# Kernel optimization log

Measured on AMD Instinct MI355X. Metric: run time of the kernel, lower is better.

The kernel has to match this reference:

```python
import jax, jax.numpy as jnp
import numpy as np
from math import sqrt

B, T, C = 4, 2048, 2048
H = 16
D = C // H  # head_dim = 128


def setup_inputs() -> dict:
    key = jax.random.key(0)
    ks = jax.random.split(key, 7)
    s = 1.0 / sqrt(C)
    return {
        "querys": jax.random.normal(ks[0], (B, T, C), dtype=jnp.float32),
        "keys": jax.random.normal(ks[1], (B, T, C), dtype=jnp.float32),
        "values": jax.random.normal(ks[2], (B, T, C), dtype=jnp.float32),
        "Wq": jax.random.normal(ks[3], (C, C), dtype=jnp.float32) * s,
        "bq": jnp.zeros((C,), dtype=jnp.float32),
        "Wk": jax.random.normal(ks[4], (C, C), dtype=jnp.float32) * s,
        "bk": jnp.zeros((C,), dtype=jnp.float32),
        "Wv": jax.random.normal(ks[5], (C, C), dtype=jnp.float32) * s,
        "bv": jnp.zeros((C,), dtype=jnp.float32),
        "Wo": jax.random.normal(ks[6], (C, C), dtype=jnp.float32) * s,
        "bo": jnp.zeros((C,), dtype=jnp.float32),
        "is_causal": 1,
    }


def reference(querys, keys, values, Wq, bq, Wk, bk, Wv, bv, Wo, bo, is_causal):
    # Linear projections: x @ W^T + b (torch nn.Linear convention), here W stored as [C_in, C_out]
    q = (querys @ Wq + bq).reshape(B, T, H, D)
    k = (keys @ Wk + bk).reshape(B, T, H, D)
    v = (values @ Wv + bv).reshape(B, T, H, D)
    # scores: [B, H, T, T]
    scores = jnp.einsum("bqhd,bkhd->bhqk", q, k) / sqrt(D)
    if is_causal:
        mask = jnp.tril(jnp.ones((T, T), dtype=bool))  # allowed positions
        scores = jnp.where(mask, scores, -jnp.inf)
    weights = jax.nn.softmax(scores, axis=-1)
    attn = jnp.einsum("bhqk,bkhd->bqhd", weights, v).reshape(B, T, C)
    return attn @ Wo + bo
```

## Files before the change

kernel.cpp:

```cpp
#include <hip/hip_runtime.h>
#include <hip/hip_bf16.h>
#include <stdint.h>

#define BB 4
#define TT 2048
#define CC 2048
#define HH 16
#define DD 128
#define MM (BB*TT)

typedef __attribute__((ext_vector_type(8))) short bh8;
typedef __attribute__((ext_vector_type(4))) float fx4;

__device__ inline ushort f2bf(float x) {
    union { float f; uint32_t u; } c; c.f = x;
    uint32_t lsb = (c.u >> 16) & 1u;
    return (ushort)((c.u + 0x7fffu + lsb) >> 16);
}

__device__ inline void async16(const void* g, void* l) {
    __builtin_amdgcn_global_load_lds(
        (const __attribute__((address_space(1))) uint32_t*)g,
        (__attribute__((address_space(3))) uint32_t*)l, 16, 0, 0);
}

__global__ __launch_bounds__(256) void convert3_k(
    const float* __restrict__ i0, const float* __restrict__ i1,
    const float* __restrict__ i2,
    ushort* __restrict__ o0, ushort* __restrict__ o1, ushort* __restrict__ o2,
    int n)
{
    const float* in; ushort* out;
    switch (blockIdx.y) {
        case 0:  in = i0; out = o0; break;
        case 1:  in = i1; out = o1; break;
        default: in = i2; out = o2; break;
    }
    int i = (int)(blockIdx.x * 256 + threadIdx.x) * 4;
    if (i + 3 < n) {
        float4 v = *(const float4*)&in[i];
        ushort4 o;
        o.x = f2bf(v.x); o.y = f2bf(v.y); o.z = f2bf(v.z); o.w = f2bf(v.w);
        *(ushort4*)&out[i] = o;
    }
}

__global__ __launch_bounds__(256) void transpose4_w_k(
    const float* __restrict__ w0, const float* __restrict__ w1,
    const float* __restrict__ w2, const float* __restrict__ w3,
    ushort* __restrict__ t0, ushort* __restrict__ t1,
    ushort* __restrict__ t2, ushort* __restrict__ t3)
{
    const float* W; ushort* Wt;
    switch (blockIdx.z) {
        case 0:  W = w0; Wt = t0; break;
        case 1:  W = w1; Wt = t1; break;
        case 2:  W = w2; Wt = t2; break;
        default: W = w3; Wt = t3; break;
    }
    __shared__ __align__(16) ushort tile[32][33];
    const int n0 = blockIdx.x * 32, k0 = blockIdx.y * 32;
    const int tx = threadIdx.x, ty = threadIdx.y;
#pragma unroll
    for (int r = 0; r < 32; r += 8)
        tile[ty + r][tx] = f2bf(W[(size_t)(k0 + ty + r) * CC + n0 + tx]);
    __syncthreads();
    const int tid = ty * 32 + tx;
    const int p = tid & 15;
    const int row = tid >> 4;
#pragma unroll
    for (int rr = 0; rr < 2; ++rr) {
        const int n_row = row + rr * 16;
        ushort2 w2;
        w2.x = tile[2 * p][n_row];
        w2.y = tile[2 * p + 1][n_row];
        *(ushort2*)&Wt[(size_t)(n0 + n_row) * CC + k0 + 2 * p] = w2;
    }
}

__global__ __launch_bounds__(256) void transpose_v_k(
    const ushort* __restrict__ V, ushort* __restrict__ Vt)
{
    __shared__ __align__(16) ushort tile[32][33];
    const int bh = blockIdx.z;
    const int b = bh >> 4, h = bh & 15;
    const int t0 = blockIdx.y * 32, d0 = blockIdx.x * 32;
    const int tx = threadIdx.x, ty = threadIdx.y;
    const ushort* Vp = V + (size_t)b * TT * CC + h * DD;
#pragma unroll
    for (int r = 0; r < 32; r += 8)
        tile[ty + r][tx] = Vp[(size_t)(t0 + ty + r) * CC + d0 + tx];
    __syncthreads();
    ushort* Vtp = Vt + (size_t)bh * DD * TT;
    const int tt = t0 + tx;
    const int p64 = (tt & ~63) | (((tt & 15) << 2) | ((tt >> 4) & 3));
#pragma unroll
    for (int r = 0; r < 32; r += 8)
        Vtp[(size_t)(d0 + ty + r) * TT + p64] = tile[tx][ty + r];
}

template<int OUTF>
__global__ __launch_bounds__(512, 2) void gemm_bf16_k(
    const ushort* __restrict__ A, const ushort* __restrict__ Bt,
    const float* __restrict__ bias, void* __restrict__ Cv, float osc)
{
    __shared__ __align__(16) char Gsm[2][65536];

    const int tid = (int)threadIdx.x;
    const int lane = tid & 63, wave = tid >> 6;
    const int fr = lane & 15, fg = lane >> 4;
    const int wm = wave >> 2, wn = wave & 3;

    const int n_tile = (int)blockIdx.x & 7;
    const int m_tile = (int)blockIdx.x >> 3;
    const int m0 = m_tile * 256, n0 = n_tile * 256;

    const ushort* Ag = A  + (size_t)m0 * CC;
    const ushort* Bg = Bt + (size_t)n0 * CC;
    const int nt = CC / 64;

    auto STAGE_G = [&](int t, int g) {
        if (t >= nt) return;
        const int khalf = g >> 1, isB = g & 1;
        char* base = Gsm[t & 1] + isB * 32768 + khalf * 16384;
        const ushort* src = isB ? Bg : Ag;
        const int kbase = t * 64 + khalf * 32;
#pragma unroll
        for (int l = 0; l < 2; ++l) {
            const int u = l * 512 + tid;
            const int j = u >> 3, s = u & 7;
            const int ek = s ^ (j & 7);
            const int e = (ek >> 2) & 1, ks = ek & 3;
            async16(src + (size_t)(2 * j + e) * CC + kbase + ks * 8,
                    base + u * 16);
        }
    };

    const int slot = ((((fr & 1) << 2) | fg) ^ ((fr >> 1) & 7));
    const int offA = (wm * 64 + (fr >> 1)) * 128 + slot * 16;
    const int offB = 32768 + (wn * 32 + (fr >> 1)) * 128 + slot * 16;

    fx4 acc[8][4];
#pragma unroll
    for (int i = 0; i < 8; ++i)
#pragma unroll
        for (int j = 0; j < 4; ++j)
            acc[i][j] = (fx4){0.f, 0.f, 0.f, 0.f};

#pragma unroll
    for (int g = 0; g < 4; ++g) STAGE_G(0, g);

#pragma unroll 1
    for (int t = 0; t < nt; ++t) {
        const char* kb = Gsm[t & 1];
#pragma unroll
        for (int kk = 0; kk < 2; ++kk) {
            if (t == nt - 1 && kk == 1) {
                asm volatile("s_waitcnt vmcnt(0)" ::: "memory");
            } else {
                asm volatile("s_waitcnt vmcnt(4)" ::: "memory");
            }
            __builtin_amdgcn_sched_barrier(0);
            __builtin_amdgcn_s_barrier();
            __builtin_amdgcn_sched_barrier(0);

            const char* ka = kb + kk * 16384;
            const char* kbB = kb + kk * 16384;
            bh8 afr[4], bfr[4];

#pragma unroll
            for (int nf = 0; nf < 4; ++nf)
                bfr[nf] = *(const bh8*)(kbB + offB + nf * 1024);
#pragma unroll
            for (int i = 0; i < 4; ++i)
                afr[i] = *(const bh8*)(ka + offA + i * 1024);
            STAGE_G(t + 1, kk * 2);

            __builtin_amdgcn_sched_barrier(0);
            __builtin_amdgcn_s_barrier();
            __builtin_amdgcn_sched_barrier(0);

            __builtin_amdgcn_s_setprio(1);
#pragma unroll
            for (int i = 0; i < 4; ++i)
#pragma unroll
                for (int nf = 0; nf < 4; ++nf)
                    acc[i][nf] = __builtin_amdgcn_mfma_f32_16x16x32_bf16(
                        afr[i], bfr[nf], acc[i][nf], 0, 0, 0);
            __builtin_amdgcn_s_setprio(0);

#pragma unroll
            for (int i = 0; i < 4; ++i)
                afr[i] = *(const bh8*)(ka + offA + (4 + i) * 1024);
            STAGE_G(t + 1, kk * 2 + 1);

            __builtin_amdgcn_sched_barrier(0);
            __builtin_amdgcn_s_barrier();
            __builtin_amdgcn_sched_barrier(0);

            __builtin_amdgcn_s_setprio(1);
#pragma unroll
            for (int i = 0; i < 4; ++i)
#pragma unroll
                for (int nf = 0; nf < 4; ++nf)
                    acc[4 + i][nf] = __builtin_amdgcn_mfma_f32_16x16x32_bf16(
                        afr[i], bfr[nf], acc[4 + i][nf], 0, 0, 0);
            __builtin_amdgcn_s_setprio(0);
        }
    }

#pragma unroll
    for (int nf = 0; nf < 4; ++nf) {
        const int col = n0 + wn * 64 + nf * 16 + fr;
        const float bv = bias[col];
#pragma unroll
        for (int mf = 0; mf < 8; ++mf) {
            const int row = m0 + wm * 128 + mf * 16 + fg * 4;
#pragma unroll
            for (int r = 0; r < 4; ++r) {
                float v = (acc[mf][nf][r] + bv) * osc;
                if (OUTF)
                    ((float*)Cv)[(size_t)(row + r) * CC + col] = v;
                else
                    ((ushort*)Cv)[(size_t)(row + r) * CC + col] = f2bf(v);
            }
        }
    }
}

__global__ __launch_bounds__(512, 4) void flash_attn_k(
    const ushort* __restrict__ Qm, const ushort* __restrict__ Km,
    const ushort* __restrict__ Vt, ushort* __restrict__ Om,
    const int* __restrict__ causal_p)
{
    __shared__ __align__(16) char Ksm[2][16384];
    __shared__ __align__(16) char Vsm[2][16384];
    __shared__ __align__(16) char Psm[8][2048];

    const int tid = (int)threadIdx.x;
    const int lane = tid & 63, wave = tid >> 6;
    const int fr = lane & 15, fg = lane >> 4;
    const int causal = causal_p[0];

    const int d_raw = (int)blockIdx.x + 8 * ((int)blockIdx.y + 16 * (int)blockIdx.z);
    const int xcd = d_raw & 7, jj = d_raw >> 3;
    const int head_lin = xcd * 8 + (jj & 7);
    const int pi = jj >> 3;
    const int h = head_lin & 15, b = head_lin >> 4;

    const ushort* Qp = Qm + (size_t)b * TT * CC + h * DD;
    const ushort* Kp = Km + (size_t)b * TT * CC + h * DD;
    const ushort* Vp = Vt + (size_t)(b * HH + h) * DD * TT;
    ushort* Op = Om + (size_t)b * TT * CC + h * DD;
    char* pl = Psm[wave];

    auto STAGE = [&](int ti, int buf) {
        const int kv0 = ti * 64;
        {
            const int r0 = tid >> 4, s0 = tid & 15;
            async16(Kp + (size_t)(kv0 + r0) * CC + (s0 ^ (r0 & 15)) * 8,
                    Ksm[buf] + tid * 16);
            async16(Kp + (size_t)(kv0 + 32 + r0) * CC + (s0 ^ (r0 & 15)) * 8,
                    Ksm[buf] + 8192 + tid * 16);
        }
        {
            const int d0 = tid >> 3, s0 = tid & 7;
            async16(Vp + (size_t)d0 * TT + kv0 + (s0 ^ (d0 & 7)) * 8,
                    Vsm[buf] + tid * 16);
            async16(Vp + (size_t)(64 + d0) * TT + kv0 + (s0 ^ (d0 & 7)) * 8,
                    Vsm[buf] + 8192 + tid * 16);
        }
    };

#pragma unroll 1
    for (int pp = 0; pp < 2; ++pp) {
        const int tile = pp ? (15 - pi) : pi;
        const int q0 = tile * 128;
        const int qbase = q0 + wave * 16;

        bh8 qf[4];
#pragma unroll
        for (int s = 0; s < 4; ++s)
            qf[s] = *(const bh8*)&Qp[(size_t)(qbase + fr) * CC + s * 32 + fg * 8];

        fx4 o[8];
#pragma unroll
        for (int jn = 0; jn < 8; ++jn) o[jn] = (fx4){0.f, 0.f, 0.f, 0.f};
        float l_r[4] = {0.f, 0.f, 0.f, 0.f};

        const int nfull  = causal ? (q0 >> 6) : (TT / 64);
        const int ntiles = causal ? (nfull + 2) : (TT / 64);

        STAGE(0, 0);
#pragma unroll 1
        for (int t = 0; t < ntiles; ++t) {
            const bool last = (t == ntiles - 1);
            if (!last) STAGE(t + 1, (t + 1) & 1);
            if (!last) { asm volatile("s_waitcnt vmcnt(4)" ::: "memory"); }
            else       { asm volatile("s_waitcnt vmcnt(0)" ::: "memory"); }
            __builtin_amdgcn_sched_barrier(0);
            __builtin_amdgcn_s_barrier();
            __builtin_amdgcn_sched_barrier(0);

            const int kv0 = t * 64;
            const char* kb = Ksm[t & 1];
            const char* vb = Vsm[t & 1];
            const bool domask = causal && (t >= nfull);
            const bool active = !domask || (kv0 <= qbase + 15);

            if (active) {
                fx4 s4[4];
#pragma unroll
                for (int j = 0; j < 4; ++j) s4[j] = (fx4){0.f, 0.f, 0.f, 0.f};
#pragma unroll
                for (int st = 0; st < 4; ++st) {
                    bh8 kf[4];
#pragma unroll
                    for (int j = 0; j < 4; ++j)
                        kf[j] = *(const bh8*)(kb + (j * 16 + fr) * 256 +
                                              ((st * 64 + fg * 16) ^ (fr << 4)));
#pragma unroll
                    for (int j = 0; j < 4; ++j)
                        s4[j] = __builtin_amdgcn_mfma_f32_16x16x32_bf16(
                            qf[st], kf[j], s4[j], 0, 0, 0);
                }

#pragma unroll
                for (int r = 0; r < 4; ++r) {
                    const int row = fg * 4 + r;
                    const int q_idx = qbase + row;
                    float pv[4];
#pragma unroll
                    for (int j = 0; j < 4; ++j) {
                        float v = s4[j][r];
                        if (domask && (kv0 + j * 16 + fr > q_idx)) v = -1e30f;
                        pv[j] = exp2f(v);
                        l_r[r] += pv[j];
                    }
                    uint w0, w1;
                    asm("v_cvt_pk_bf16_f32 %0, %1, %2"
                        : "=v"(w0) : "v"(pv[0]), "v"(pv[1]));
                    asm("v_cvt_pk_bf16_f32 %0, %1, %2"
                        : "=v"(w1) : "v"(pv[2]), "v"(pv[3]));
                    uint2 w2; w2.x = w0; w2.y = w1;
                    *(uint2*)(pl + row * 128 + ((fr * 8) ^ ((row & 7) << 4))) = w2;
                }

#pragma unroll
                for (int g = 0; g < 2; ++g) {
                    bh8 pf = *(const bh8*)(pl + fr * 128 +
                                           ((g * 64 + fg * 16) ^ ((fr & 7) << 4)));
#pragma unroll
                    for (int jn = 0; jn < 8; ++jn) {
                        bh8 vf = *(const bh8*)(vb + (jn * 16 + fr) * 128 +
                                               ((g * 64 + fg * 16) ^ ((fr & 7) << 4)));
                        o[jn] = __builtin_amdgcn_mfma_f32_16x16x32_bf16(
                            pf, vf, o[jn], 0, 0, 0);
                    }
                }
            }

            __builtin_amdgcn_sched_barrier(0);
            __builtin_amdgcn_s_barrier();
            __builtin_amdgcn_sched_barrier(0);
        }

#pragma unroll
        for (int r = 0; r < 4; ++r) {
            float l = l_r[r];
            l += __shfl_xor(l, 1, 16);
            l += __shfl_xor(l, 2, 16);
            l += __shfl_xor(l, 4, 16);
            l += __shfl_xor(l, 8, 16);
            l_r[r] = l;
        }

#pragma unroll
        for (int r = 0; r < 4; ++r) {
            const float inv = 1.0f / l_r[r];
            const size_t rowoff = (size_t)(qbase + fg * 4 + r) * CC;
#pragma unroll
            for (int jn = 0; jn < 8; ++jn)
                Op[rowoff + jn * 16 + fr] = f2bf(o[jn][r] * inv);
        }
    }
}

extern "C" void kernel_launch(void* const* d_in, const int* in_sizes, int n_in,
                              void* d_out, int out_size, void* d_ws, size_t ws_size,
                              hipStream_t stream)
{
    (void)in_sizes; (void)n_in; (void)out_size;
    const float* querys = (const float*)d_in[0];
    const float* keys   = (const float*)d_in[1];
    const float* values = (const float*)d_in[2];
    const float* Wq = (const float*)d_in[3];
    const float* bq = (const float*)d_in[4];
    const float* Wk = (const float*)d_in[5];
    const float* bk = (const float*)d_in[6];
    const float* Wv = (const float*)d_in[7];
    const float* bv = (const float*)d_in[8];
    const float* Wo = (const float*)d_in[9];
    const float* bo = (const float*)d_in[10];
    const int* is_causal = (const int*)d_in[11];

    const size_t WBYTES = (size_t)CC * CC * 2;
    const size_t XBYTES = (size_t)MM * CC * 2;
    if (ws_size < 4 * WBYTES + 4 * XBYTES) return;

    uint8_t* ws = (uint8_t*)d_ws;
    ushort* WqT = (ushort*)(ws);
    ushort* WkT = (ushort*)(ws + WBYTES);
    ushort* WvT = (ushort*)(ws + 2 * WBYTES);
    ushort* WoT = (ushort*)(ws + 3 * WBYTES);
    uint8_t* act = ws + 4 * WBYTES;
    ushort* Xq = (ushort*)(act);
    ushort* Xk = (ushort*)(act + XBYTES);
    ushort* Xv = (ushort*)(act + 2 * XBYTES);
    ushort* Qb = (ushort*)(act + 3 * XBYTES);
    ushort* Kb = Xq;
    ushort* Vb = Xk;
    ushort* Vt = Xv;
    ushort* Ob = Xk;

    dim3 tb(32, 8);
    transpose4_w_k<<<dim3(CC / 32, CC / 32, 4), tb, 0, stream>>>(
        Wq, Wk, Wv, Wo, WqT, WkT, WvT, WoT);

    const int nX = MM * CC;
    convert3_k<<<dim3(nX / 4 / 256, 3), 256, 0, stream>>>(
        querys, keys, values, Xq, Xk, Xv, nX);

    dim3 gg((MM / 256) * (CC / 256));

    const float QSC = 0.12751789836306614f;

    gemm_bf16_k<0><<<gg, 512, 0, stream>>>(Xq, WqT, bq, Qb, QSC);
    gemm_bf16_k<0><<<gg, 512, 0, stream>>>(Xk, WkT, bk, Kb, 1.0f);
    gemm_bf16_k<0><<<gg, 512, 0, stream>>>(Xv, WvT, bv, Vb, 1.0f);

    dim3 gvt(DD / 32, TT / 32, BB * HH);
    transpose_v_k<<<gvt, tb, 0, stream>>>(Vb, Vt);

    dim3 ga(8, HH, BB);
    flash_attn_k<<<ga, 512, 0, stream>>>(Qb, Kb, Vt, Ob, is_causal);

    gemm_bf16_k<1><<<gg, 512, 0, stream>>>(Ob, WoT, bo, d_out, 1.0f);
}
```

Baseline: 528.7 us.

## Compute transposed S so P stays in registers, dropping LDS round-trip

```diff
diff --git a/kernel.cpp b/kernel.cpp
--- a/kernel.cpp
+++ b/kernel.cpp
@@ -93,10 +93,10 @@
     __syncthreads();
     ushort* Vtp = Vt + (size_t)bh * DD * TT;
     const int tt = t0 + tx;
-    const int p64 = (tt & ~63) | (((tt & 15) << 2) | ((tt >> 4) & 3));
+    const int pnew = (tt & ~31) | (((tt >> 2) & 3) << 3) | (((tt >> 4) & 1) << 2) | (tt & 3);
 #pragma unroll
     for (int r = 0; r < 32; r += 8)
-        Vtp[(size_t)(d0 + ty + r) * TT + p64] = tile[tx][ty + r];
+        Vtp[(size_t)(d0 + ty + r) * TT + pnew] = tile[tx][ty + r];
 }
 
 template<int OUTF>
@@ -235,7 +235,6 @@
 {
     __shared__ __align__(16) char Ksm[2][16384];
     __shared__ __align__(16) char Vsm[2][16384];
-    __shared__ __align__(16) char Psm[8][2048];
 
     const int tid = (int)threadIdx.x;
     const int lane = tid & 63, wave = tid >> 6;
@@ -252,7 +251,6 @@
     const ushort* Kp = Km + (size_t)b * TT * CC + h * DD;
     const ushort* Vp = Vt + (size_t)(b * HH + h) * DD * TT;
     ushort* Op = Om + (size_t)b * TT * CC + h * DD;
-    char* pl = Psm[wave];
 
     auto STAGE = [&](int ti, int buf) {
         const int kv0 = ti * 64;
@@ -277,6 +275,7 @@
         const int tile = pp ? (15 - pi) : pi;
         const int q0 = tile * 128;
         const int qbase = q0 + wave * 16;
+        const int q_idx = qbase + fr;
 
         bh8 qf[4];
 #pragma unroll
@@ -286,7 +285,7 @@
         fx4 o[8];
 #pragma unroll
         for (int jn = 0; jn < 8; ++jn) o[jn] = (fx4){0.f, 0.f, 0.f, 0.f};
-        float l_r[4] = {0.f, 0.f, 0.f, 0.f};
+        float l_acc = 0.f;
 
         const int nfull  = causal ? (q0 >> 6) : (TT / 64);
         const int ntiles = causal ? (nfull + 2) : (TT / 64);
@@ -312,6 +311,7 @@
                 fx4 s4[4];
 #pragma unroll
                 for (int j = 0; j < 4; ++j) s4[j] = (fx4){0.f, 0.f, 0.f, 0.f};
+                __builtin_amdgcn_s_setprio(1);
 #pragma unroll
                 for (int st = 0; st < 4; ++st) {
                     bh8 kf[4];
@@ -322,34 +322,37 @@
 #pragma unroll
                     for (int j = 0; j < 4; ++j)
                         s4[j] = __builtin_amdgcn_mfma_f32_16x16x32_bf16(
-                            qf[st], kf[j], s4[j], 0, 0, 0);
+                            kf[j], qf[st], s4[j], 0, 0, 0);
                 }
-
-#pragma unroll
-                for (int r = 0; r < 4; ++r) {
-                    const int row = fg * 4 + r;
-                    const int q_idx = qbase + row;
-                    float pv[4];
-#pragma unroll
-                    for (int j = 0; j < 4; ++j) {
-                        float v = s4[j][r];
-                        if (domask && (kv0 + j * 16 + fr > q_idx)) v = -1e30f;
-                        pv[j] = exp2f(v);
-                        l_r[r] += pv[j];
+                __builtin_amdgcn_s_setprio(0);
+
+#pragma unroll
+                for (int g = 0; g < 2; ++g) {
+                    float pg[2][4];
+#pragma unroll
+                    for (int j2 = 0; j2 < 2; ++j2) {
+                        const int jb = g * 2 + j2;
+#pragma unroll
+                        for (int r = 0; r < 4; ++r) {
+                            float v = s4[jb][r];
+                            if (domask && (kv0 + jb * 16 + fg * 4 + r > q_idx))
+                                v = -1e30f;
+                            pg[j2][r] = exp2f(v);
+                        }
+                        l_acc += (pg[j2][0] + pg[j2][1]) + (pg[j2][2] + pg[j2][3]);
                     }
-                    uint w0, w1;
+                    union { uint u[4]; bh8 h; } pk;
                     asm("v_cvt_pk_bf16_f32 %0, %1, %2"
-                        : "=v"(w0) : "v"(pv[0]), "v"(pv[1]));
+                        : "=v"(pk.u[0]) : "v"(pg[0][0]), "v"(pg[0][1]));
                     asm("v_cvt_pk_bf16_f32 %0, %1, %2"
-                        : "=v"(w1) : "v"(pv[2]), "v"(pv[3]));
-                    uint2 w2; w2.x = w0; w2.y = w1;
-                    *(uint2*)(pl + row * 128 + ((fr * 8) ^ ((row & 7) << 4))) = w2;
-                }
-
-#pragma unroll
-                for (int g = 0; g < 2; ++g) {
-                    bh8 pf = *(const bh8*)(pl + fr * 128 +
-                                           ((g * 64 + fg * 16) ^ ((fr & 7) << 4)));
+                        : "=v"(pk.u[1]) : "v"(pg[0][2]), "v"(pg[0][3]));
+                    asm("v_cvt_pk_bf16_f32 %0, %1, %2"
+                        : "=v"(pk.u[2]) : "v"(pg[1][0]), "v"(pg[1][1]));
+                    asm("v_cvt_pk_bf16_f32 %0, %1, %2"
+                        : "=v"(pk.u[3]) : "v"(pg[1][2]), "v"(pg[1][3]));
+                    const bh8 pf = pk.h;
+
+                    __builtin_amdgcn_s_setprio(1);
 #pragma unroll
                     for (int jn = 0; jn < 8; ++jn) {
                         bh8 vf = *(const bh8*)(vb + (jn * 16 + fr) * 128 +
@@ -357,6 +360,7 @@
                         o[jn] = __builtin_amdgcn_mfma_f32_16x16x32_bf16(
                             pf, vf, o[jn], 0, 0, 0);
                     }
+                    __builtin_amdgcn_s_setprio(0);
                 }
             }
 
@@ -365,19 +369,13 @@
             __builtin_amdgcn_sched_barrier(0);
         }
 
+        float lsum = l_acc;
+        lsum += __shfl_xor(lsum, 16);
+        lsum += __shfl_xor(lsum, 32);
+
 #pragma unroll
         for (int r = 0; r < 4; ++r) {
-            float l = l_r[r];
-            l += __shfl_xor(l, 1, 16);
-            l += __shfl_xor(l, 2, 16);
-            l += __shfl_xor(l, 4, 16);
-            l += __shfl_xor(l, 8, 16);
-            l_r[r] = l;
-        }
-
-#pragma unroll
-        for (int r = 0; r < 4; ++r) {
-            const float inv = 1.0f / l_r[r];
+            const float inv = 1.0f / __shfl(lsum, fg * 4 + r, 16);
             const size_t rowoff = (size_t)(qbase + fg * 4 + r) * CC;
 #pragma unroll
             for (int jn = 0; jn < 8; ++jn)
```

New measurement: 509.1 us. -3.7%, faster.
